# Kernel tuning notes

Measured on AMD Instinct MI355X. Metric: run time of the kernel, lower is better.

## Reference

```python
import jax, jax.numpy as jnp
import numpy as np

LN_EPS = 1e-3  # keras LayerNormalization default
HEADS_GAT = 4

def _gelu(x):
    return jax.nn.gelu(x, approximate=False)  # keras 'gelu' is exact

def _ln(x, g, b):
    m = jnp.mean(x, axis=-1, keepdims=True)
    v = jnp.var(x, axis=-1, keepdims=True)
    return (x - m) / jnp.sqrt(v + LN_EPS) * g + b

def _gat(x, mask, w, a_src, a_dst, bias, heads):
    # dense-masked GAT: attention restricted to adj > 0.5 (self-loops present
    # since cosine-sim diagonal is 1). x: [BS, N, F]
    BS, N, _ = x.shape
    D = w.shape[1] // heads
    h = (x @ w).reshape(BS, N, heads, D)
    es = jnp.einsum('bnhd,hd->bnh', h, a_src)  # source term
    ed = jnp.einsum('bnhd,hd->bnh', h, a_dst)  # destination term
    # e[b,i,j,h]: edge j -> i
    e = jax.nn.leaky_relu(ed[:, :, None, :] + es[:, None, :, :], 0.2)
    e = jnp.where(mask[None, :, :, None], e, -1e9)
    alpha = jax.nn.softmax(e, axis=2)  # softmax over sources j
    out = jnp.einsum('bijh,bjhd->bihd', alpha, h).reshape(BS, N, heads * D)
    return out + bias

def _mha(x, wq, bq, wk, bk, wv, bv, wo, bo):
    q = jnp.einsum('bsf,fhd->bshd', x, wq) + bq
    k = jnp.einsum('bsf,fhd->bshd', x, wk) + bk
    v = jnp.einsum('bsf,fhd->bshd', x, wv) + bv
    s = jnp.einsum('bshd,bthd->bhst', q, k) / jnp.sqrt(jnp.asarray(q.shape[-1], x.dtype))
    a = jax.nn.softmax(s, axis=-1)
    o = jnp.einsum('bhst,bthd->bshd', a, v)
    return jnp.einsum('bshd,hdf->bsf', o, wo) + bo

def setup_inputs() -> dict:
    key = jax.random.key(0)
    ks = jax.random.split(key, 40)
    B, S, N = 4, 16, 400
    HID, OUT, DM, MH, DK, FF = 16, 32, 32, 2, 16, 64
    f32 = jnp.float32
    def glorot(k, shape, fin, fout):
        return jax.random.normal(k, shape, f32) * np.sqrt(2.0 / (fin + fout)).astype(np.float32)
    return {
        'x': jax.random.normal(ks[0], (B, S, N, 3), f32),
        'adj_embed': glorot(ks[1], (N, HID), N, HID),
        'proj_w': glorot(ks[2], (3, HID), 3, HID), 'proj_b': jnp.zeros((HID,), f32),
        'g1_w': glorot(ks[3], (HID, HID), HID, HID),
        'g1_asrc': glorot(ks[4], (4, HID // 4), HID, 4), 'g1_adst': glorot(ks[5], (4, HID // 4), HID, 4),
        'g1_b': jnp.zeros((HID,), f32),
        'g2_w': glorot(ks[6], (HID, OUT), HID, OUT),
        'g2_asrc': glorot(ks[7], (4, OUT // 4), OUT, 4), 'g2_adst': glorot(ks[8], (4, OUT // 4), OUT, 4),
        'g2_b': jnp.zeros((OUT,), f32),
        'wq': glorot(ks[9], (DM, MH, DK), DM, DM), 'bq': jnp.zeros((MH, DK), f32),
        'wk': glorot(ks[10], (DM, MH, DK), DM, DM), 'bk': jnp.zeros((MH, DK), f32),
        'wv': glorot(ks[11], (DM, MH, DK), DM, DM), 'bv': jnp.zeros((MH, DK), f32),
        'wo': glorot(ks[12], (MH, DK, DM), DM, DM), 'bo': jnp.zeros((DM,), f32),
        'ln1_g': jnp.ones((DM,), f32), 'ln1_b': jnp.zeros((DM,), f32),
        'f_w1': glorot(ks[13], (DM, FF), DM, FF), 'f_b1': jnp.zeros((FF,), f32),
        'f_w2': glorot(ks[14], (FF, DM), FF, DM), 'f_b2': jnp.zeros((DM,), f32),
        'ln2_g': jnp.ones((DM,), f32), 'ln2_b': jnp.zeros((DM,), f32),
        'r_w1': glorot(ks[15], (DM, 16), DM, 16), 'r_b1': jnp.zeros((16,), f32),
        'r_w2': glorot(ks[16], (16, 1), 16, 1), 'r_b2': jnp.zeros((1,), f32),
    }

def reference(x, adj_embed, proj_w, proj_b, g1_w, g1_asrc, g1_adst, g1_b,
              g2_w, g2_asrc, g2_adst, g2_b, wq, bq, wk, bk, wv, bv, wo, bo,
              ln1_g, ln1_b, f_w1, f_b1, f_w2, f_b2, ln2_g, ln2_b,
              r_w1, r_b1, r_w2, r_b2):
    B, S, N, _ = x.shape
    DM = 32
    xs = x.reshape(B * S, N, 3)
    # adaptive adjacency: cosine similarity of learned node embeddings
    emb = adj_embed / jnp.sqrt(jnp.maximum(jnp.sum(adj_embed * adj_embed, -1, keepdims=True), 1e-12))
    mask = (emb @ emb.T) > 0.5  # [N, N], shared across batch
    h = xs @ proj_w + proj_b
    h = _gelu(_gat(h, mask, g1_w, g1_asrc, g1_adst, g1_b, HEADS_GAT))
    h = _gat(h, mask, g2_w, g2_asrc, g2_adst, g2_b, HEADS_GAT)  # [B*S, N, 32]
    # faithful to source: plain reshape (no transpose) into temporal batch
    t = h.reshape(B, S, N, DM).reshape(B * N, S, DM)
    attn = _mha(t, wq, bq, wk, bk, wv, bv, wo, bo)
    t = _ln(t + attn, ln1_g, ln1_b)
    f = _gelu(t @ f_w1 + f_b1) @ f_w2 + f_b2
    t = _ln(t + f, ln2_g, ln2_b)
    t = t.reshape(B, N, S, DM)
    m = jnp.mean(t, axis=2)  # [B, N, 32]
    r = _gelu(m @ r_w1 + r_b1) @ r_w2 + r_b2
    return r[..., 0]  # [B, N]
```

## Files before the change

### kernel.cpp

```cpp
#include <hip/hip_runtime.h>

#define DEVINL __device__ __forceinline__

DEVINL float gelu_exact(float x){ return 0.5f * x * (1.0f + erff(x * 0.70710678118654752f)); }
DEVINL float lrelu02(float x){ return x >= 0.0f ? x : 0.2f * x; }

#define NN    400
#define NROWS 25600
#define NSEQ  1600

#define OFF_NBR  0u
#define OFF_CNT  320000u
#define OFF_HP1  321600u
#define OFF_ES1  1960000u
#define OFF_ED1  2369600u
#define OFF_HP2  2779200u
#define OFF_ES2  6056000u
#define OFF_ED2  6465600u

__global__ __launch_bounds__(256) void k_nbr_pre1(const float* __restrict__ emb,
    const float* __restrict__ x, const float* __restrict__ pw, const float* __restrict__ pb,
    const float* __restrict__ g1w, const float* __restrict__ as1, const float* __restrict__ ad1,
    unsigned short* __restrict__ nlist, int* __restrict__ cnt,
    float* __restrict__ hp1, float* __restrict__ es1, float* __restrict__ ed1){
  if (blockIdx.x < NN){
    const int i = blockIdx.x;
    const int lane = threadIdx.x;
    if (lane >= 64) return;
    double ai[16];
    double si = 0.0;
    #pragma unroll
    for (int k = 0; k < 16; k++){ ai[k] = (double)emb[i*16 + k]; si += ai[k]*ai[k]; }
    const double rni = 1.0 / sqrt(fmax(si, 1e-12));
    int base = 0;
    #pragma unroll
    for (int t = 0; t < 7; t++){
      const int j = t*64 + lane;
      bool valid = false;
      if (j < NN){
        double sj = 0.0, dp = 0.0;
        #pragma unroll
        for (int k = 0; k < 16; k++){
          double bv = (double)emb[j*16 + k];
          sj += bv*bv; dp += ai[k]*bv;
        }
        double c = dp * rni / sqrt(fmax(sj, 1e-12));
        valid = (c > 0.5);
      }
      unsigned long long bal = __ballot(valid);
      int pre = __popcll(bal & ((1ull << lane) - 1ull));
      if (valid) nlist[i*NN + base + pre] = (unsigned short)j;
      base += (int)__popcll(bal);
    }
    if (lane == 0) cnt[i] = base;
    return;
  }
  __shared__ float s_pw[48], s_pb[16], s_w[256], s_as[16], s_ad[16];
  const int tid = threadIdx.x;
  if (tid < 48) s_pw[tid] = pw[tid];
  if (tid < 16){ s_pb[tid] = pb[tid]; s_as[tid] = as1[tid]; s_ad[tid] = ad1[tid]; }
  s_w[tid] = g1w[tid];
  __syncthreads();
  const int row = (blockIdx.x - NN) * 256 + tid;
  if (row >= NROWS) return;
  float x0 = x[row*3+0], x1v = x[row*3+1], x2 = x[row*3+2];
  float h0[16];
  #pragma unroll
  for (int c = 0; c < 16; c++)
    h0[c] = s_pb[c] + x0 * s_pw[c] + x1v * s_pw[16+c] + x2 * s_pw[32+c];
  float hp[16];
  #pragma unroll
  for (int c = 0; c < 16; c++){
    float a = 0.f;
    #pragma unroll
    for (int k = 0; k < 16; k++) a += h0[k] * s_w[k*16 + c];
    hp[c] = a;
  }
  float4* hout = (float4*)(hp1 + (size_t)row * 16);
  hout[0] = make_float4(hp[0],hp[1],hp[2],hp[3]);
  hout[1] = make_float4(hp[4],hp[5],hp[6],hp[7]);
  hout[2] = make_float4(hp[8],hp[9],hp[10],hp[11]);
  hout[3] = make_float4(hp[12],hp[13],hp[14],hp[15]);
  #pragma unroll
  for (int h = 0; h < 4; h++){
    float es = 0.f, ed = 0.f;
    #pragma unroll
    for (int d = 0; d < 4; d++){ es += hp[h*4+d]*s_as[h*4+d]; ed += hp[h*4+d]*s_ad[h*4+d]; }
    es1[row*4 + h] = es;
    ed1[row*4 + h] = ed;
  }
}

__global__ __launch_bounds__(256) void k_gat1pre2(
    const float* __restrict__ hp1, const float* __restrict__ es1, const float* __restrict__ ed1,
    const unsigned short* __restrict__ nlist, const int* __restrict__ cnt,
    const float* __restrict__ g1b, const float* __restrict__ g2w,
    const float* __restrict__ as2, const float* __restrict__ ad2,
    float* __restrict__ hp2, float* __restrict__ es2, float* __restrict__ ed2){
  __shared__ float s_w[512], s_b1[16], s_as[32], s_ad[32];
  const int tid = threadIdx.x;
  s_w[tid] = g2w[tid]; s_w[tid+256] = g2w[tid+256];
  if (tid < 16) s_b1[tid] = g1b[tid];
  if (tid < 32){ s_as[tid] = as2[tid]; s_ad[tid] = ad2[tid]; }
  __syncthreads();
  const int row = blockIdx.x * 256 + tid;
  if (row >= NROWS) return;
  const int gb = row / NN;
  const int i  = row - gb * NN;
  const int n  = cnt[i];
  const unsigned short* nl = nlist + i * NN;
  const float4* esb = (const float4*)(es1 + (size_t)gb * NN * 4);
  const float*  hpb = hp1 + (size_t)gb * NN * 16;
  const float4 edv = *(const float4*)(ed1 + (size_t)row * 4);
  const float edr[4] = {edv.x, edv.y, edv.z, edv.w};
  float mx[4] = {-1e30f,-1e30f,-1e30f,-1e30f};
  for (int k0 = 0; k0 < n; k0 += 8){
    int jj[8]; float wv[8];
    #pragma unroll
    for (int u = 0; u < 8; u++){
      int kk = k0+u; jj[u] = (int)nl[kk < n ? kk : n-1]; wv[u] = (kk < n) ? 1.f : 0.f;
    }
    #pragma unroll
    for (int u = 0; u < 8; u++){
      float4 e4 = esb[jj[u]];
      mx[0] = fmaxf(mx[0], wv[u] > 0.5f ? e4.x : -1e30f);
      mx[1] = fmaxf(mx[1], wv[u] > 0.5f ? e4.y : -1e30f);
      mx[2] = fmaxf(mx[2], wv[u] > 0.5f ? e4.z : -1e30f);
      mx[3] = fmaxf(mx[3], wv[u] > 0.5f ? e4.w : -1e30f);
    }
  }
  float m[4];
  #pragma unroll
  for (int h = 0; h < 4; h++) m[h] = lrelu02(edr[h] + mx[h]);
  float den[4] = {0.f,0.f,0.f,0.f};
  float acc[16];
  #pragma unroll
  for (int d = 0; d < 16; d++) acc[d] = 0.f;
  for (int k0 = 0; k0 < n; k0 += 8){
    int jj[8]; float wv[8];
    #pragma unroll
    for (int u = 0; u < 8; u++){
      int kk = k0+u; jj[u] = (int)nl[kk < n ? kk : n-1]; wv[u] = (kk < n) ? 1.f : 0.f;
    }
    #pragma unroll
    for (int u = 0; u < 8; u++){
      float4 e4 = esb[jj[u]];
      const float4* hv = (const float4*)(hpb + (size_t)jj[u] * 16);
      float4 h0 = hv[0], h1 = hv[1], h2v = hv[2], h3 = hv[3];
      float p0 = wv[u] * __expf(lrelu02(edr[0]+e4.x) - m[0]); den[0] += p0;
      float p1 = wv[u] * __expf(lrelu02(edr[1]+e4.y) - m[1]); den[1] += p1;
      float p2 = wv[u] * __expf(lrelu02(edr[2]+e4.z) - m[2]); den[2] += p2;
      float p3 = wv[u] * __expf(lrelu02(edr[3]+e4.w) - m[3]); den[3] += p3;
      acc[0]  += p0*h0.x;  acc[1]  += p0*h0.y;  acc[2]  += p0*h0.z;  acc[3]  += p0*h0.w;
      acc[4]  += p1*h1.x;  acc[5]  += p1*h1.y;  acc[6]  += p1*h1.z;  acc[7]  += p1*h1.w;
      acc[8]  += p2*h2v.x; acc[9]  += p2*h2v.y; acc[10] += p2*h2v.z; acc[11] += p2*h2v.w;
      acc[12] += p3*h3.x;  acc[13] += p3*h3.y;  acc[14] += p3*h3.z;  acc[15] += p3*h3.w;
    }
  }
  float x1r[16];
  #pragma unroll
  for (int h = 0; h < 4; h++){
    float inv = 1.0f / den[h];
    #pragma unroll
    for (int d = 0; d < 4; d++)
      x1r[h*4+d] = gelu_exact(acc[h*4+d] * inv + s_b1[h*4+d]);
  }
  float hp[32];
  #pragma unroll
  for (int c = 0; c < 32; c++){
    float a = 0.f;
    #pragma unroll
    for (int k = 0; k < 16; k++) a += x1r[k] * s_w[k*32 + c];
    hp[c] = a;
  }
  float4* ho = (float4*)(hp2 + (size_t)row * 32);
  #pragma unroll
  for (int qd = 0; qd < 8; qd++)
    ho[qd] = make_float4(hp[qd*4], hp[qd*4+1], hp[qd*4+2], hp[qd*4+3]);
  #pragma unroll
  for (int h = 0; h < 4; h++){
    float es = 0.f, ed = 0.f;
    #pragma unroll
    for (int d = 0; d < 8; d++){ es += hp[h*8+d]*s_as[h*8+d]; ed += hp[h*8+d]*s_ad[h*8+d]; }
    es2[row*4 + h] = es;
    ed2[row*4 + h] = ed;
  }
}

struct TW { const float* p[20]; };

__global__ __launch_bounds__(256) void k_trans7(
    const float* __restrict__ hp2, const float* __restrict__ es2,
    const float* __restrict__ ed2, const unsigned short* __restrict__ nlist,
    const int* __restrict__ cnt, const float* __restrict__ g2b,
    TW tw, float* __restrict__ out){
  __shared__ float Wq[1024], Wk[1024], Wv[1024], Wo[1024];
  __shared__ float Fw1[2048], Fw2[2048], Rw1[512];
  __shared__ float Bq[32], Bk[32], Bv[32], Bo[32], L1g[32], L1b[32];
  __shared__ float Fb1[64], Fb2[32], L2g[32], L2b[32], Rb1v[16], Rw2[16];
  __shared__ float Gb2[32];
  __shared__ float Rb2s[1];
  __shared__ float SCR[4][2640];
  const int tid = threadIdx.x;
  const int w = tid >> 6, lane = tid & 63;
  for (int i = tid; i < 1024; i += 256){
    Wq[i] = tw.p[0][i]; Wk[i] = tw.p[2][i]; Wv[i] = tw.p[4][i]; Wo[i] = tw.p[6][i];
  }
  for (int i = tid; i < 2048; i += 256){ Fw1[i] = tw.p[10][i]; Fw2[i] = tw.p[12][i]; }
  for (int i = tid; i < 512; i += 256) Rw1[i] = tw.p[16][i];
  if (tid < 32){
    Bq[tid] = tw.p[1][tid]; Bk[tid] = tw.p[3][tid]; Bv[tid] = tw.p[5][tid]; Bo[tid] = tw.p[7][tid];
    L1g[tid] = tw.p[8][tid]; L1b[tid] = tw.p[9][tid]; Fb2[tid] = tw.p[13][tid];
    L2g[tid] = tw.p[14][tid]; L2b[tid] = tw.p[15][tid];
    Gb2[tid] = g2b[tid];
  }
  if (tid < 64) Fb1[tid] = tw.p[11][tid];
  if (tid < 16){ Rb1v[tid] = tw.p[17][tid]; Rw2[tid] = tw.p[18][tid]; }
  if (tid == 0) Rb2s[0] = tw.p[19][0];
  __syncthreads();

  float* Tw = SCR[w];
  float* Kw = Tw + 528;
  float* Vw = Tw + 1056;
  float* Sw = Tw + 1584;
  const int p = blockIdx.x * 4 + w;
  const int s = lane >> 2, cg = lane & 3, ob = cg * 8;

  {
    const int r  = p * 16 + s;
    const int gb = r / NN;
    const int i  = r - gb * NN;
    const int n  = cnt[i];
    const unsigned short* nl = nlist + i * NN;
    const int rbase = gb * NN;
    const float edh = ed2[(size_t)r * 4 + cg];
    float mx = -1e30f;
    for (int k0 = 0; k0 < n; k0 += 8){
      int jj[8]; float wv[8];
      #pragma unroll
      for (int u = 0; u < 8; u++){
        int kk = k0+u; jj[u] = (int)nl[kk < n ? kk : n-1]; wv[u] = (kk < n) ? 1.f : 0.f;
      }
      #pragma unroll
      for (int u = 0; u < 8; u++){
        float v = es2[(size_t)(rbase + jj[u]) * 4 + cg];
        mx = fmaxf(mx, wv[u] > 0.5f ? v : -1e30f);
      }
    }
    const float m = lrelu02(edh + mx);
    float den = 0.f;
    float acc[8];
    #pragma unroll
    for (int d = 0; d < 8; d++) acc[d] = 0.f;
    for (int k0 = 0; k0 < n; k0 += 8){
      int jj[8]; float wv[8], ev[8];
      #pragma unroll
      for (int u = 0; u < 8; u++){
        int kk = k0+u; jj[u] = (int)nl[kk < n ? kk : n-1]; wv[u] = (kk < n) ? 1.f : 0.f;
      }
      #pragma unroll
      for (int u = 0; u < 8; u++) ev[u] = es2[(size_t)(rbase + jj[u]) * 4 + cg];
      #pragma unroll
      for (int u = 0; u < 8; u++){
        float pv = wv[u] * __expf(lrelu02(edh + ev[u]) - m);
        den += pv;
        const float4* vp = (const float4*)(hp2 + (size_t)(rbase + jj[u]) * 32 + cg * 8);
        float4 v0 = vp[0], v1 = vp[1];
        acc[0] += pv*v0.x; acc[1] += pv*v0.y; acc[2] += pv*v0.z; acc[3] += pv*v0.w;
        acc[4] += pv*v1.x; acc[5] += pv*v1.y; acc[6] += pv*v1.z; acc[7] += pv*v1.w;
      }
    }
    const float invd = 1.0f / den;
    float* tr = Tw + s*33 + ob;
    #pragma unroll
    for (int u = 0; u < 8; u++) tr[u] = acc[u] * invd + Gb2[ob + u];
  }
  float q[8], kk[8], vv[8];
  #pragma unroll
  for (int u = 0; u < 8; u++){ q[u] = Bq[ob+u]; kk[u] = Bk[ob+u]; vv[u] = Bv[ob+u]; }
  for (int f = 0; f < 32; f++){
    float tv = Tw[s*33 + f];
    #pragma unroll
    for (int u = 0; u < 8; u++){
      q[u]  += tv * Wq[f*32 + ob + u];
      kk[u] += tv * Wk[f*32 + ob + u];
      vv[u] += tv * Wv[f*32 + ob + u];
    }
  }
  #pragma unroll
  for (int u = 0; u < 8; u++){
    Sw[s*33 + ob + u] = q[u];
    Kw[s*33 + ob + u] = kk[u];
    Vw[s*33 + ob + u] = vv[u];
  }
  const int ai = (lane >> 1) & 15;
  const int hb = (lane >> 5) * 16 + (lane & 1) * 8;
  float qreg[8];
  #pragma unroll
  for (int u = 0; u < 8; u++) qreg[u] = Sw[ai*33 + hb + u];
  float sc[16];
  float mx = -1e30f;
  #pragma unroll
  for (int j = 0; j < 16; j++){
    float d = 0.f;
    #pragma unroll
    for (int u = 0; u < 8; u++) d += qreg[u] * Kw[j*33 + hb + u];
    d += __shfl_xor(d, 1);
    d *= 0.25f;
    sc[j] = d;
    mx = fmaxf(mx, d);
  }
  float den = 0.f;
  #pragma unroll
  for (int j = 0; j < 16; j++){ sc[j] = __expf(sc[j] - mx); den += sc[j]; }
  const float ainv = 1.0f / den;
  float at[8];
  #pragma unroll
  for (int u = 0; u < 8; u++) at[u] = 0.f;
  #pragma unroll
  for (int j = 0; j < 16; j++){
    float al = sc[j];
    #pragma unroll
    for (int u = 0; u < 8; u++) at[u] += al * Vw[j*33 + hb + u];
  }
  #pragma unroll
  for (int u = 0; u < 8; u++) Sw[ai*33 + hb + u] = at[u] * ainv;
  float xr[8];
  #pragma unroll
  for (int u = 0; u < 8; u++) xr[u] = Bo[ob + u];
  for (int i2 = 0; i2 < 32; i2++){
    float av = Sw[s*33 + i2];
    #pragma unroll
    for (int u = 0; u < 8; u++) xr[u] += av * Wo[i2*32 + ob + u];
  }
  #pragma unroll
  for (int u = 0; u < 8; u++) xr[u] += Tw[s*33 + ob + u];
  float sm = 0.f, sq = 0.f;
  #pragma unroll
  for (int u = 0; u < 8; u++){ sm += xr[u]; sq += xr[u]*xr[u]; }
  sm += __shfl_xor(sm, 1); sq += __shfl_xor(sq, 1);
  sm += __shfl_xor(sm, 2); sq += __shfl_xor(sq, 2);
  {
    float mean = sm * (1.f/32.f);
    float var  = sq * (1.f/32.f) - mean*mean;
    float rinv = 1.0f / sqrtf(var + 1e-3f);
    #pragma unroll
    for (int u = 0; u < 8; u++)
      Tw[s*33 + ob + u] = (xr[u] - mean) * rinv * L1g[ob+u] + L1b[ob+u];
  }
  {
    const int cb = cg * 16;
    #pragma unroll
    for (int t = 0; t < 16; t++){
      int c = cb + t;
      float a = Fb1[c];
      for (int f = 0; f < 32; f++) a += Tw[s*33 + f] * Fw1[f*64 + c];
      Sw[s*66 + c] = gelu_exact(a);
    }
  }
  float y[8];
  #pragma unroll
  for (int u = 0; u < 8; u++) y[u] = Fb2[ob + u];
  for (int c = 0; c < 64; c++){
    float fv = Sw[s*66 + c];
    #pragma unroll
    for (int u = 0; u < 8; u++) y[u] += fv * Fw2[c*32 + ob + u];
  }
  #pragma unroll
  for (int u = 0; u < 8; u++) y[u] += Tw[s*33 + ob + u];
  sm = 0.f; sq = 0.f;
  #pragma unroll
  for (int u = 0; u < 8; u++){ sm += y[u]; sq += y[u]*y[u]; }
  sm += __shfl_xor(sm, 1); sq += __shfl_xor(sq, 1);
  sm += __shfl_xor(sm, 2); sq += __shfl_xor(sq, 2);
  float mean2 = sm * (1.f/32.f);
  float var2  = sq * (1.f/32.f) - mean2*mean2;
  float rinv2 = 1.0f / sqrtf(var2 + 1e-3f);
  float mv[8];
  #pragma unroll
  for (int u = 0; u < 8; u++){
    float v = (y[u] - mean2) * rinv2 * L2g[ob+u] + L2b[ob+u];
    v += __shfl_xor(v, 4);  v += __shfl_xor(v, 8);
    v += __shfl_xor(v, 16); v += __shfl_xor(v, 32);
    mv[u] = v * (1.f/16.f);
  }
  if (s == 0){
    #pragma unroll
    for (int u = 0; u < 8; u++) Tw[ob + u] = mv[u];
  }
  const int t = lane & 15;
  float hid = Rb1v[t];
  for (int o2 = 0; o2 < 32; o2++) hid += Tw[o2] * Rw1[o2*16 + t];
  hid = gelu_exact(hid) * Rw2[t];
  hid += __shfl_xor(hid, 1); hid += __shfl_xor(hid, 2);
  hid += __shfl_xor(hid, 4); hid += __shfl_xor(hid, 8);
  if (lane == 0) out[p] = hid + Rb2s[0];
}

extern "C" void kernel_launch(void* const* d_in, const int* in_sizes, int n_in,
                              void* d_out, int out_size, void* d_ws, size_t ws_size,
                              hipStream_t stream){
  const float* x    = (const float*)d_in[0];
  const float* adj  = (const float*)d_in[1];
  const float* pw   = (const float*)d_in[2];
  const float* pb   = (const float*)d_in[3];
  const float* g1w  = (const float*)d_in[4];
  const float* g1as = (const float*)d_in[5];
  const float* g1ad = (const float*)d_in[6];
  const float* g1b  = (const float*)d_in[7];
  const float* g2w  = (const float*)d_in[8];
  const float* g2as = (const float*)d_in[9];
  const float* g2ad = (const float*)d_in[10];
  const float* g2b  = (const float*)d_in[11];

  char* ws = (char*)d_ws;
  unsigned short* nlist = (unsigned short*)(ws + OFF_NBR);
  int*   cnt = (int*)(ws + OFF_CNT);
  float* hp1 = (float*)(ws + OFF_HP1);
  float* es1 = (float*)(ws + OFF_ES1);
  float* ed1 = (float*)(ws + OFF_ED1);
  float* hp2 = (float*)(ws + OFF_HP2);
  float* es2 = (float*)(ws + OFF_ES2);
  float* ed2 = (float*)(ws + OFF_ED2);

  TW tw;
  for (int t = 0; t < 20; t++) tw.p[t] = (const float*)d_in[12 + t];

  hipLaunchKernelGGL(k_nbr_pre1, dim3(NN + 100), dim3(256), 0, stream,
                     adj, x, pw, pb, g1w, g1as, g1ad, nlist, cnt, hp1, es1, ed1);
  hipLaunchKernelGGL(k_gat1pre2, dim3(100), dim3(256), 0, stream,
                     hp1, es1, ed1, nlist, cnt, g1b, g2w, g2as, g2ad, hp2, es2, ed2);
  hipLaunchKernelGGL(k_trans7, dim3(NSEQ/4), dim3(256), 0, stream,
                     hp2, es2, ed2, nlist, cnt, g2b, tw, (float*)d_out);
}
```

Baseline: 64.86 us.

## Split GAT1 aggregation across four threads per row, one per head

The GAT layer-1 aggregation kernel now assigns four threads to each node row, one per attention head, instead of one thread per row. This raises the grid from 100 to 400 blocks, which improves occupancy and latency hiding on a GPU with many CUs. The per-head results go through a small shared-memory tile so each thread can compute its 8-column slice of the layer-2 projection and the matching es/ed terms. In exchange, the neighbor list and index loads are repeated four times, and each gather reads narrower, less coalesced values.

```diff
diff --git a/kernel.cpp b/kernel.cpp
--- a/kernel.cpp
+++ b/kernel.cpp
@@ -98,22 +98,21 @@
     const float* __restrict__ as2, const float* __restrict__ ad2,
     float* __restrict__ hp2, float* __restrict__ es2, float* __restrict__ ed2){
   __shared__ float s_w[512], s_b1[16], s_as[32], s_ad[32];
+  __shared__ float x1s[64][17];
   const int tid = threadIdx.x;
   s_w[tid] = g2w[tid]; s_w[tid+256] = g2w[tid+256];
   if (tid < 16) s_b1[tid] = g1b[tid];
   if (tid < 32){ s_as[tid] = as2[tid]; s_ad[tid] = ad2[tid]; }
   __syncthreads();
-  const int row = blockIdx.x * 256 + tid;
-  if (row >= NROWS) return;
+  const int lrow = tid >> 2, h = tid & 3;
+  const int row = blockIdx.x * 64 + lrow;
   const int gb = row / NN;
   const int i  = row - gb * NN;
   const int n  = cnt[i];
   const unsigned short* nl = nlist + i * NN;
-  const float4* esb = (const float4*)(es1 + (size_t)gb * NN * 4);
-  const float*  hpb = hp1 + (size_t)gb * NN * 16;
-  const float4 edv = *(const float4*)(ed1 + (size_t)row * 4);
-  const float edr[4] = {edv.x, edv.y, edv.z, edv.w};
-  float mx[4] = {-1e30f,-1e30f,-1e30f,-1e30f};
+  const int rbase = gb * NN;
+  const float edh = ed1[(size_t)row * 4 + h];
+  float mx = -1e30f;
   for (int k0 = 0; k0 < n; k0 += 8){
     int jj[8]; float wv[8];
     #pragma unroll
@@ -122,69 +121,54 @@
     }
     #pragma unroll
     for (int u = 0; u < 8; u++){
-      float4 e4 = esb[jj[u]];
-      mx[0] = fmaxf(mx[0], wv[u] > 0.5f ? e4.x : -1e30f);
-      mx[1] = fmaxf(mx[1], wv[u] > 0.5f ? e4.y : -1e30f);
-      mx[2] = fmaxf(mx[2], wv[u] > 0.5f ? e4.z : -1e30f);
-      mx[3] = fmaxf(mx[3], wv[u] > 0.5f ? e4.w : -1e30f);
-    }
-  }
-  float m[4];
-  #pragma unroll
-  for (int h = 0; h < 4; h++) m[h] = lrelu02(edr[h] + mx[h]);
-  float den[4] = {0.f,0.f,0.f,0.f};
-  float acc[16];
-  #pragma unroll
-  for (int d = 0; d < 16; d++) acc[d] = 0.f;
+      float v = es1[(size_t)(rbase + jj[u]) * 4 + h];
+      mx = fmaxf(mx, wv[u] > 0.5f ? v : -1e30f);
+    }
+  }
+  const float m = lrelu02(edh + mx);
+  float den = 0.f;
+  float acc[4] = {0.f, 0.f, 0.f, 0.f};
   for (int k0 = 0; k0 < n; k0 += 8){
-    int jj[8]; float wv[8];
+    int jj[8]; float wv[8], ev[8];
     #pragma unroll
     for (int u = 0; u < 8; u++){
       int kk = k0+u; jj[u] = (int)nl[kk < n ? kk : n-1]; wv[u] = (kk < n) ? 1.f : 0.f;
     }
     #pragma unroll
+    for (int u = 0; u < 8; u++) ev[u] = es1[(size_t)(rbase + jj[u]) * 4 + h];
+    #pragma unroll
     for (int u = 0; u < 8; u++){
-      float4 e4 = esb[jj[u]];
-      const float4* hv = (const float4*)(hpb + (size_t)jj[u] * 16);
-      float4 h0 = hv[0], h1 = hv[1], h2v = hv[2], h3 = hv[3];
-      float p0 = wv[u] * __expf(lrelu02(edr[0]+e4.x) - m[0]); den[0] += p0;
-      float p1 = wv[u] * __expf(lrelu02(edr[1]+e4.y) - m[1]); den[1] += p1;
-      float p2 = wv[u] * __expf(lrelu02(edr[2]+e4.z) - m[2]); den[2] += p2;
-      float p3 = wv[u] * __expf(lrelu02(edr[3]+e4.w) - m[3]); den[3] += p3;
-      acc[0]  += p0*h0.x;  acc[1]  += p0*h0.y;  acc[2]  += p0*h0.z;  acc[3]  += p0*h0.w;
-      acc[4]  += p1*h1.x;  acc[5]  += p1*h1.y;  acc[6]  += p1*h1.z;  acc[7]  += p1*h1.w;
-      acc[8]  += p2*h2v.x; acc[9]  += p2*h2v.y; acc[10] += p2*h2v.z; acc[11] += p2*h2v.w;
-      acc[12] += p3*h3.x;  acc[13] += p3*h3.y;  acc[14] += p3*h3.z;  acc[15] += p3*h3.w;
-    }
-  }
-  float x1r[16];
-  #pragma unroll
-  for (int h = 0; h < 4; h++){
-    float inv = 1.0f / den[h];
-    #pragma unroll
-    for (int d = 0; d < 4; d++)
-      x1r[h*4+d] = gelu_exact(acc[h*4+d] * inv + s_b1[h*4+d]);
-  }
-  float hp[32];
-  #pragma unroll
-  for (int c = 0; c < 32; c++){
+      float pv = wv[u] * __expf(lrelu02(edh + ev[u]) - m);
+      den += pv;
+      float4 hv = *(const float4*)(hp1 + (size_t)(rbase + jj[u]) * 16 + h * 4);
+      acc[0] += pv*hv.x; acc[1] += pv*hv.y; acc[2] += pv*hv.z; acc[3] += pv*hv.w;
+    }
+  }
+  const float inv = 1.0f / den;
+  #pragma unroll
+  for (int d = 0; d < 4; d++)
+    x1s[lrow][h*4 + d] = gelu_exact(acc[d] * inv + s_b1[h*4 + d]);
+  __syncthreads();
+  float xr[16];
+  #pragma unroll
+  for (int k = 0; k < 16; k++) xr[k] = x1s[lrow][k];
+  const int cb = h * 8;
+  float hp[8];
+  #pragma unroll
+  for (int c = 0; c < 8; c++){
     float a = 0.f;
     #pragma unroll
-    for (int k = 0; k < 16; k++) a += x1r[k] * s_w[k*32 + c];
+    for (int k = 0; k < 16; k++) a += xr[k] * s_w[k*32 + cb + c];
     hp[c] = a;
   }
-  float4* ho = (float4*)(hp2 + (size_t)row * 32);
-  #pragma unroll
-  for (int qd = 0; qd < 8; qd++)
-    ho[qd] = make_float4(hp[qd*4], hp[qd*4+1], hp[qd*4+2], hp[qd*4+3]);
-  #pragma unroll
-  for (int h = 0; h < 4; h++){
-    float es = 0.f, ed = 0.f;
-    #pragma unroll
-    for (int d = 0; d < 8; d++){ es += hp[h*8+d]*s_as[h*8+d]; ed += hp[h*8+d]*s_ad[h*8+d]; }
-    es2[row*4 + h] = es;
-    ed2[row*4 + h] = ed;
-  }
+  float4* ho = (float4*)(hp2 + (size_t)row * 32 + cb);
+  ho[0] = make_float4(hp[0], hp[1], hp[2], hp[3]);
+  ho[1] = make_float4(hp[4], hp[5], hp[6], hp[7]);
+  float es = 0.f, ed = 0.f;
+  #pragma unroll
+  for (int d = 0; d < 8; d++){ es += hp[d]*s_as[cb+d]; ed += hp[d]*s_ad[cb+d]; }
+  es2[(size_t)row*4 + h] = es;
+  ed2[(size_t)row*4 + h] = ed;
 }
 
 struct TW { const float* p[20]; };
@@ -428,7 +412,7 @@
 
   hipLaunchKernelGGL(k_nbr_pre1, dim3(NN + 100), dim3(256), 0, stream,
                      adj, x, pw, pb, g1w, g1as, g1ad, nlist, cnt, hp1, es1, ed1);
-  hipLaunchKernelGGL(k_gat1pre2, dim3(100), dim3(256), 0, stream,
+  hipLaunchKernelGGL(k_gat1pre2, dim3(NROWS/64), dim3(256), 0, stream,
                      hp1, es1, ed1, nlist, cnt, g1b, g2w, g2as, g2ad, hp2, es2, ed2);
   hipLaunchKernelGGL(k_trans7, dim3(NSEQ/4), dim3(256), 0, stream,
                      hp2, es2, ed2, nlist, cnt, g2b, tw, (float*)d_out);
```

Result: faster. 58.35 us (-10.0%).
